# Optimization experiments

Hardware: AMD Instinct MI355X
Metric: run time of the kernel (lower is better)

## Reference

```python
import jax, jax.numpy as jnp
import numpy as np

N_NODES = 50000
N_EDGES = 1_600_000
IN_CH, HID_CH, OUT_CH, EDGE_DIM = 128, 128, 64, 16
NEG_SLOPE = 0.2


def _glorot(key, shape):
    fan = sum(shape) if len(shape) > 1 else shape[0] + 1
    lim = jnp.sqrt(6.0 / fan)
    return jax.random.uniform(key, shape, jnp.float32, -lim, lim)


def setup_inputs() -> dict:
    key = jax.random.key(0)
    ks = jax.random.split(key, 16)
    x = jax.random.normal(ks[0], (N_NODES, IN_CH), jnp.float32)
    edge_index = jax.random.randint(ks[1], (2, N_EDGES), 0, N_NODES, jnp.int32)
    flepe = jax.random.normal(ks[2], (N_EDGES, EDGE_DIM), jnp.float32)
    # layer 1 params (GATConv heads=1)
    W1 = _glorot(ks[3], (IN_CH, HID_CH))
    att_src1 = _glorot(ks[4], (HID_CH,))
    att_dst1 = _glorot(ks[5], (HID_CH,))
    We1 = _glorot(ks[6], (EDGE_DIM, HID_CH))
    att_edge1 = _glorot(ks[7], (HID_CH,))
    b1 = jnp.zeros((HID_CH,), jnp.float32)
    # layer 2 params
    W2 = _glorot(ks[8], (HID_CH, OUT_CH))
    att_src2 = _glorot(ks[9], (OUT_CH,))
    att_dst2 = _glorot(ks[10], (OUT_CH,))
    We2 = _glorot(ks[11], (EDGE_DIM, OUT_CH))
    att_edge2 = _glorot(ks[12], (OUT_CH,))
    b2 = jnp.zeros((OUT_CH,), jnp.float32)
    return {"x": x, "edge_index": edge_index, "flepe": flepe,
            "W1": W1, "att_src1": att_src1, "att_dst1": att_dst1,
            "We1": We1, "att_edge1": att_edge1, "b1": b1,
            "W2": W2, "att_src2": att_src2, "att_dst2": att_dst2,
            "We2": We2, "att_edge2": att_edge2, "b2": b2}


def gat_conv(x, src, dst, edge_attr, W, a_s, a_d, We, a_e, b, n_nodes):
    # PyG GATConv, heads=1, concat=True, negative_slope=0.2, edge_dim set.
    h = x @ W                                    # [N, C]
    alpha_src = h @ a_s                          # [N]
    alpha_dst = h @ a_d                          # [N]
    e = edge_attr @ We                           # [E, C]
    alpha_edge = e @ a_e                         # [E]
    alpha = alpha_src[src] + alpha_dst[dst] + alpha_edge
    alpha = jax.nn.leaky_relu(alpha, NEG_SLOPE)  # [E]
    # segment softmax over incoming edges per destination node
    amax = jax.ops.segment_max(alpha, dst, num_segments=n_nodes)
    amax = jnp.where(jnp.isfinite(amax), amax, 0.0)
    ex = jnp.exp(alpha - amax[dst])
    denom = jax.ops.segment_sum(ex, dst, num_segments=n_nodes)
    coef = ex / (denom[dst] + 1e-16)
    out = jax.ops.segment_sum(coef[:, None] * h[src], dst, num_segments=n_nodes)
    return out + b


def reference(x, edge_index, flepe,
              W1, att_src1, att_dst1, We1, att_edge1, b1,
              W2, att_src2, att_dst2, We2, att_edge2, b2):
    src, dst = edge_index[0], edge_index[1]
    n = x.shape[0]
    # dropout(p=0.5) is identity in eval mode
    h = gat_conv(x, src, dst, flepe, W1, att_src1, att_dst1, We1, att_edge1, b1, n)
    h = jax.nn.relu(h)
    out = gat_conv(h, src, dst, flepe, W2, att_src2, att_dst2, We2, att_edge2, b2, n)
    return out
```

## Files before the change

kernel.cpp:

```cpp
#include <hip/hip_runtime.h>
#include <hip/hip_bf16.h>

typedef unsigned int uint;


__device__ inline float bf2f_lo(uint u) { return __uint_as_float((u & 0xffffu) << 16); }
__device__ inline float bf2f_hi(uint u) { return __uint_as_float(u & 0xffff0000u); }
__device__ inline uint f2bf_rne(float f) {
    uint x = __float_as_uint(f);
    return (x + 0x7fffu + ((x >> 16) & 1u)) >> 16;
}
__device__ inline uint pack_bf2(float a, float b) { return f2bf_rne(a) | (f2bf_rne(b) << 16); }

__global__ void k_deg(const int* __restrict__ dst, int* __restrict__ deg, int E,
                      const float* __restrict__ We1, const float* __restrict__ ae1w,
                      const float* __restrict__ We2, const float* __restrict__ ae2w,
                      float* __restrict__ p1, float* __restrict__ p2) {
    if (blockIdx.x == 0) {
        int t = threadIdx.x;
        if (t < 16) {
            float s = 0.f;
            for (int c = 0; c < 128; ++c) s += We1[t * 128 + c] * ae1w[c];
            p1[t] = s;
        } else if (t < 32) {
            int d = t - 16;
            float s = 0.f;
            for (int c = 0; c < 64; ++c) s += We2[d * 64 + c] * ae2w[c];
            p2[d] = s;
        }
    }
    int e = blockIdx.x * blockDim.x + threadIdx.x;
    if (e < E) atomicAdd(&deg[dst[e]], 1);
}

__global__ __launch_bounds__(1024) void k_scanA(const int* __restrict__ deg,
                                                int* __restrict__ excl,
                                                int* __restrict__ bsum, int N) {
    __shared__ int s[1024];
    int tid = threadIdx.x;
    int gid = blockIdx.x * 1024 + tid;
    int v = (gid < N) ? deg[gid] : 0;
    s[tid] = v;
    __syncthreads();
    for (int off = 1; off < 1024; off <<= 1) {
        int t = (tid >= off) ? s[tid - off] : 0;
        __syncthreads();
        s[tid] += t;
        __syncthreads();
    }
    if (gid < N) excl[gid] = s[tid] - v;
    if (tid == 1023) bsum[blockIdx.x] = s[1023];
}

__global__ void k_scanB(const int* __restrict__ bsum, int* __restrict__ bsumx, int nb,
                        int* __restrict__ rowstart, int N, int E) {
    int t = threadIdx.x;
    int v = (t < nb) ? bsum[t] : 0;
    int x = v;
    for (int o = 1; o < 64; o <<= 1) {
        int y = __shfl_up(x, o);
        if (t >= o) x += y;
    }
    if (t < nb) bsumx[t] = x - v;
    if (t == 0) rowstart[N] = E;
}

__global__ __launch_bounds__(1024) void k_scanC(const int* __restrict__ excl,
                                                const int* __restrict__ bsumx,
                                                int* __restrict__ rowstart,
                                                int* __restrict__ cursor, int N) {
    int gid = blockIdx.x * 1024 + threadIdx.x;
    if (gid < N) {
        int v = excl[gid] + bsumx[blockIdx.x];
        rowstart[gid] = v;
        cursor[gid] = v;
    }
}

__global__ void k_scat(const int* __restrict__ src, const int* __restrict__ dst,
                       const float* __restrict__ fe,
                       const float* __restrict__ p1, const float* __restrict__ p2,
                       int* __restrict__ cursor, float4* __restrict__ rec, int E) {
    float q1[16], q2[16];
#pragma unroll
    for (int i = 0; i < 16; ++i) { q1[i] = p1[i]; q2[i] = p2[i]; }
    int e = blockIdx.x * blockDim.x + threadIdx.x;
    if (e >= E) return;
    int s = src[e], d = dst[e];
    const float4* f = reinterpret_cast<const float4*>(fe) + (size_t)e * 4;
    float a1 = 0.f, a2 = 0.f;
#pragma unroll
    for (int j = 0; j < 4; ++j) {
        float4 v = f[j];
        a1 += v.x * q1[4 * j] + v.y * q1[4 * j + 1] + v.z * q1[4 * j + 2] + v.w * q1[4 * j + 3];
        a2 += v.x * q2[4 * j] + v.y * q2[4 * j + 1] + v.z * q2[4 * j + 2] + v.w * q2[4 * j + 3];
    }
    int pos = atomicAdd(&cursor[d], 1);
    rec[pos] = make_float4(__int_as_float(s), a1, a2, 0.f);
}

template <int COUT>
__global__ __launch_bounds__(256) void k_gemm(
    const float* __restrict__ X, const float* __restrict__ W,
    const float* __restrict__ avs, const float* __restrict__ avd,
    uint* __restrict__ Hb, float* __restrict__ asrc, float* __restrict__ adst, int N) {
    __shared__ float Wl[128 * COUT];
    const int tid = threadIdx.x;
    {
        const float4* W4 = reinterpret_cast<const float4*>(W);
        float4* Wl4 = reinterpret_cast<float4*>(Wl);
        for (int i = tid; i < 128 * COUT / 4; i += 256) Wl4[i] = W4[i];
    }
    __syncthreads();
    const int wv = tid >> 6, lane = tid & 63;
    const int base = __builtin_amdgcn_readfirstlane(blockIdx.x * 32 + wv * 8);

    const float4* xr[8];
#pragma unroll
    for (int r = 0; r < 8; ++r) {
        int g = base + r;
        if (g > N - 1) g = N - 1;
        xr[r] = reinterpret_cast<const float4*>(X + (size_t)g * 128);
    }
    float acc[8][2];
#pragma unroll
    for (int r = 0; r < 8; ++r) { acc[r][0] = 0.f; acc[r][1] = 0.f; }

    for (int k4 = 0; k4 < 32; ++k4) {
        float xv[8][4];
#pragma unroll
        for (int r = 0; r < 8; ++r) {
            float4 t = xr[r][k4];
            xv[r][0] = t.x; xv[r][1] = t.y; xv[r][2] = t.z; xv[r][3] = t.w;
        }
#pragma unroll
        for (int kk = 0; kk < 4; ++kk) {
            int k = 4 * k4 + kk;
            if constexpr (COUT == 128) {
                float2 w2 = *reinterpret_cast<const float2*>(&Wl[k * 128 + 2 * lane]);
#pragma unroll
                for (int r = 0; r < 8; ++r) {
                    acc[r][0] = fmaf(xv[r][kk], w2.x, acc[r][0]);
                    acc[r][1] = fmaf(xv[r][kk], w2.y, acc[r][1]);
                }
            } else {
                float w1 = Wl[k * COUT + lane];
#pragma unroll
                for (int r = 0; r < 8; ++r)
                    acc[r][0] = fmaf(xv[r][kk], w1, acc[r][0]);
            }
        }
    }

#pragma unroll
    for (int r = 0; r < 8; ++r) {
        int g = base + r;
        if (g < N) {
            if constexpr (COUT == 128) {
                Hb[(size_t)g * 64 + lane] = pack_bf2(acc[r][0], acc[r][1]);
                float2 s2 = reinterpret_cast<const float2*>(avs)[lane];
                float2 d2 = reinterpret_cast<const float2*>(avd)[lane];
                float ps = acc[r][0] * s2.x + acc[r][1] * s2.y;
                float pd = acc[r][0] * d2.x + acc[r][1] * d2.y;
                for (int o = 32; o; o >>= 1) { ps += __shfl_xor(ps, o); pd += __shfl_xor(pd, o); }
                if (lane == 0) { asrc[g] = ps; adst[g] = pd; }
            } else {
                float partner = __shfl_xor(acc[r][0], 1);
                if ((lane & 1) == 0)
                    Hb[(size_t)g * 32 + (lane >> 1)] = pack_bf2(acc[r][0], partner);
                float ps = acc[r][0] * avs[lane];
                float pd = acc[r][0] * avd[lane];
                for (int o = 32; o; o >>= 1) { ps += __shfl_xor(ps, o); pd += __shfl_xor(pd, o); }
                if (lane == 0) { asrc[g] = ps; adst[g] = pd; }
            }
        }
    }
}

__global__ __launch_bounds__(256) void k_aggr1(
    const int* __restrict__ rowstart, const float4* __restrict__ rec,
    const float* __restrict__ asrc, const float* __restrict__ adst,
    const uint* __restrict__ Hb, const float* __restrict__ bias,
    float* __restrict__ out, int N) {
    __shared__ uint2 swl[4][64];
    const int wv = threadIdx.x >> 6, lane = threadIdx.x & 63;
    int n = blockIdx.x * 4 + wv;
    if (n >= N) return;
    n = __builtin_amdgcn_readfirstlane(n);
    int s = rowstart[n], e = rowstart[n + 1];
    float ad = adst[n];
    float a0 = 0.f, a1 = 0.f, ws = 0.f;
    for (int base = s; base < e; base += 64) {
        int cnt = e - base; if (cnt > 64) cnt = 64;
        float w = 0.f; int sn = 0;
        if (lane < cnt) {
            float4 rc = rec[base + lane];
            sn = __float_as_int(rc.x);
            float al = asrc[sn] + ad + rc.y;
            al = al > 0.f ? al : 0.2f * al;
            w = __expf(al);
        }
        float wsum = w;
        for (int o = 32; o; o >>= 1) wsum += __shfl_xor(wsum, o);
        ws += wsum;
        swl[wv][lane] = make_uint2((uint)sn, __float_as_uint(w));
        int cnt4 = (cnt + 3) & ~3;
        for (int j = 0; j < cnt4; j += 4) {
            uint2 t0 = swl[wv][j], t1 = swl[wv][j + 1], t2 = swl[wv][j + 2], t3 = swl[wv][j + 3];
            uint h0 = Hb[(size_t)t0.x * 64 + lane];
            uint h1 = Hb[(size_t)t1.x * 64 + lane];
            uint h2 = Hb[(size_t)t2.x * 64 + lane];
            uint h3 = Hb[(size_t)t3.x * 64 + lane];
            float w0 = __uint_as_float(t0.y), w1 = __uint_as_float(t1.y);
            float w2 = __uint_as_float(t2.y), w3 = __uint_as_float(t3.y);
            a0 = fmaf(w0, bf2f_lo(h0), a0); a1 = fmaf(w0, bf2f_hi(h0), a1);
            a0 = fmaf(w1, bf2f_lo(h1), a0); a1 = fmaf(w1, bf2f_hi(h1), a1);
            a0 = fmaf(w2, bf2f_lo(h2), a0); a1 = fmaf(w2, bf2f_hi(h2), a1);
            a0 = fmaf(w3, bf2f_lo(h3), a0); a1 = fmaf(w3, bf2f_hi(h3), a1);
        }
    }
    float inv = 1.0f / (ws + 1e-16f);
    float2 b2 = reinterpret_cast<const float2*>(bias)[lane];
    float o0 = fmaxf(fmaf(a0, inv, b2.x), 0.f);
    float o1 = fmaxf(fmaf(a1, inv, b2.y), 0.f);
    reinterpret_cast<float2*>(out)[(size_t)n * 64 + lane] = make_float2(o0, o1);
}

__global__ __launch_bounds__(256) void k_aggr2(
    const int* __restrict__ rowstart, const float4* __restrict__ rec,
    const float* __restrict__ asrc, const float* __restrict__ adst,
    const uint* __restrict__ Hb, const float* __restrict__ bias,
    float* __restrict__ out, int N) {
    __shared__ uint2 swl[4][64];
    const int wv = threadIdx.x >> 6, lane = threadIdx.x & 63;
    const int half = lane >> 5, hl = lane & 31;
    int n = blockIdx.x * 4 + wv;
    if (n >= N) return;
    n = __builtin_amdgcn_readfirstlane(n);
    int s = rowstart[n], e = rowstart[n + 1];
    float ad = adst[n];
    float a0 = 0.f, a1 = 0.f, ws = 0.f;
    for (int base = s; base < e; base += 64) {
        int cnt = e - base; if (cnt > 64) cnt = 64;
        float w = 0.f; int sn = 0;
        if (lane < cnt) {
            float4 rc = rec[base + lane];
            sn = __float_as_int(rc.x);
            float al = asrc[sn] + ad + rc.z;
            al = al > 0.f ? al : 0.2f * al;
            w = __expf(al);
        }
        float wsum = w;
        for (int o = 32; o; o >>= 1) wsum += __shfl_xor(wsum, o);
        ws += wsum;
        swl[wv][lane] = make_uint2((uint)sn, __float_as_uint(w));
        int cnt4 = (cnt + 3) & ~3;
        for (int j = 0; j < cnt4; j += 4) {
            uint2 t0 = swl[wv][j + half];
            uint2 t1 = swl[wv][j + 2 + half];
            uint h0 = Hb[(size_t)t0.x * 32 + hl];
            uint h1 = Hb[(size_t)t1.x * 32 + hl];
            float w0 = __uint_as_float(t0.y), w1 = __uint_as_float(t1.y);
            a0 = fmaf(w0, bf2f_lo(h0), a0); a1 = fmaf(w0, bf2f_hi(h0), a1);
            a0 = fmaf(w1, bf2f_lo(h1), a0); a1 = fmaf(w1, bf2f_hi(h1), a1);
        }
    }
    a0 += __shfl_xor(a0, 32);
    a1 += __shfl_xor(a1, 32);
    if (half == 0) {
        float inv = 1.0f / (ws + 1e-16f);
        float2 b2 = reinterpret_cast<const float2*>(bias)[hl];
        reinterpret_cast<float2*>(out)[(size_t)n * 32 + hl] =
            make_float2(fmaf(a0, inv, b2.x), fmaf(a1, inv, b2.y));
    }
}

extern "C" void kernel_launch(void* const* d_in, const int* in_sizes, int n_in,
                              void* d_out, int out_size, void* d_ws, size_t ws_size,
                              hipStream_t stream) {
    const float* x    = (const float*)d_in[0];
    const int*   ei   = (const int*)d_in[1];
    const float* fe   = (const float*)d_in[2];
    const float* W1   = (const float*)d_in[3];
    const float* as1  = (const float*)d_in[4];
    const float* ad1  = (const float*)d_in[5];
    const float* We1  = (const float*)d_in[6];
    const float* ae1w = (const float*)d_in[7];
    const float* b1   = (const float*)d_in[8];
    const float* W2   = (const float*)d_in[9];
    const float* as2  = (const float*)d_in[10];
    const float* ad2  = (const float*)d_in[11];
    const float* We2  = (const float*)d_in[12];
    const float* ae2w = (const float*)d_in[13];
    const float* b2   = (const float*)d_in[14];
    float* out = (float*)d_out;

    const int N = in_sizes[0] / 128;
    const int E = in_sizes[1] / 2;
    const int* src = ei;
    const int* dst = ei + E;

    char* ws = (char*)d_ws;
    size_t off = 0;
    auto alloc = [&](size_t bytes) -> void* {
        void* p = ws + off;
        off = (off + bytes + 255) & ~(size_t)255;
        return p;
    };
    float*  p1       = (float*)alloc(64);
    float*  p2       = (float*)alloc(64);
    float4* rec      = (float4*)alloc((size_t)E * 16);
    float*  x2       = (float*)alloc((size_t)N * 128 * 4);
    uint*   H1       = (uint*)alloc((size_t)N * 64 * 4);
    uint*   H2       = (uint*)alloc((size_t)N * 32 * 4);
    float*  asrc     = (float*)alloc((size_t)N * 4);
    float*  adst     = (float*)alloc((size_t)N * 4);
    int*    deg      = (int*)alloc((size_t)N * 4);
    int*    excl     = (int*)alloc((size_t)N * 4);
    int*    rowstart = (int*)alloc((size_t)(N + 1) * 4);
    int*    cursor   = (int*)alloc((size_t)N * 4);
    int*    bsum     = (int*)alloc(256);
    int*    bsumx    = (int*)alloc(256);

    const int nb = (N + 1023) / 1024;

    hipMemsetAsync(deg, 0, (size_t)N * 4, stream);
    k_deg<<<(E + 255) / 256, 256, 0, stream>>>(dst, deg, E, We1, ae1w, We2, ae2w, p1, p2);
    k_scanA<<<nb, 1024, 0, stream>>>(deg, excl, bsum, N);
    k_scanB<<<1, 64, 0, stream>>>(bsum, bsumx, nb, rowstart, N, E);
    k_scanC<<<nb, 1024, 0, stream>>>(excl, bsumx, rowstart, cursor, N);
    k_scat<<<(E + 255) / 256, 256, 0, stream>>>(src, dst, fe, p1, p2, cursor, rec, E);

    k_gemm<128><<<(N + 31) / 32, 256, 0, stream>>>(x, W1, as1, ad1, H1, asrc, adst, N);
    k_aggr1<<<(N + 3) / 4, 256, 0, stream>>>(rowstart, rec, asrc, adst, H1, b1, x2, N);

    k_gemm<64><<<(N + 31) / 32, 256, 0, stream>>>(x2, W2, as2, ad2, H2, asrc, adst, N);
    k_aggr2<<<(N + 3) / 4, 256, 0, stream>>>(rowstart, rec, asrc, adst, H2, b2, out, N);
}
```

Measured before the change: 542.8 us.

## Use bf16 MFMA for node GEMMs and store layer-1 output as bf16

Replaces the scalar fp32 FMA GEMMs with MFMA 16x16x32 bf16 kernels that read pre-swizzled bf16 weight fragments built by a new prep kernel. The attention projections are reduced from the MFMA accumulators. The layer-1 aggregation now writes bf16 instead of fp32, which halves traffic for the intermediate and feeds the second GEMM directly. In exchange the inputs lose precision to bf16. With N=50000, which is a multiple of 16, the tiled rows need no bounds check, but other sizes would read and write past the end.

```diff
diff --git a/kernel.cpp b/kernel.cpp
--- a/kernel.cpp
+++ b/kernel.cpp
@@ -2,6 +2,8 @@
 #include <hip/hip_bf16.h>
 
 typedef unsigned int uint;
+typedef __attribute__((ext_vector_type(8))) short bf16x8;
+typedef __attribute__((ext_vector_type(4))) float f32x4;
 
 
 __device__ inline float bf2f_lo(uint u) { return __uint_as_float((u & 0xffffu) << 16); }
@@ -11,6 +13,31 @@
     return (x + 0x7fffu + ((x >> 16) & 1u)) >> 16;
 }
 __device__ inline uint pack_bf2(float a, float b) { return f2bf_rne(a) | (f2bf_rne(b) << 16); }
+
+__global__ void k_prep(const float* __restrict__ W1, const float* __restrict__ W2,
+                       uint4* __restrict__ S1, uint4* __restrict__ S2) {
+    int t = blockIdx.x * 256 + threadIdx.x;
+    if (t < 2048) {
+        int f = t >> 6, l = t & 63;
+        int kb = f >> 3, cb = f & 7;
+        int k0 = kb * 32 + (l >> 4) * 8, c = cb * 16 + (l & 15);
+        uint u[4];
+#pragma unroll
+        for (int m = 0; m < 4; ++m)
+            u[m] = pack_bf2(W1[(k0 + 2 * m) * 128 + c], W1[(k0 + 2 * m + 1) * 128 + c]);
+        S1[t] = make_uint4(u[0], u[1], u[2], u[3]);
+    } else if (t < 3072) {
+        int tt = t - 2048;
+        int f = tt >> 6, l = tt & 63;
+        int kb = f >> 2, cb = f & 3;
+        int k0 = kb * 32 + (l >> 4) * 8, c = cb * 16 + (l & 15);
+        uint u[4];
+#pragma unroll
+        for (int m = 0; m < 4; ++m)
+            u[m] = pack_bf2(W2[(k0 + 2 * m) * 64 + c], W2[(k0 + 2 * m + 1) * 64 + c]);
+        S2[tt] = make_uint4(u[0], u[1], u[2], u[3]);
+    }
+}
 
 __global__ void k_deg(const int* __restrict__ dst, int* __restrict__ deg, int E,
                       const float* __restrict__ We1, const float* __restrict__ ae1w,
@@ -99,80 +126,89 @@
     rec[pos] = make_float4(__int_as_float(s), a1, a2, 0.f);
 }
 
-template <int COUT>
-__global__ __launch_bounds__(256) void k_gemm(
-    const float* __restrict__ X, const float* __restrict__ W,
+template <int COUT, bool BF16IN>
+__global__ __launch_bounds__(256) void k_gemm_mfma(
+    const void* __restrict__ Xv, const uint4* __restrict__ Wswz,
     const float* __restrict__ avs, const float* __restrict__ avd,
-    uint* __restrict__ Hb, float* __restrict__ asrc, float* __restrict__ adst, int N) {
-    __shared__ float Wl[128 * COUT];
-    const int tid = threadIdx.x;
-    {
-        const float4* W4 = reinterpret_cast<const float4*>(W);
-        float4* Wl4 = reinterpret_cast<float4*>(Wl);
-        for (int i = tid; i < 128 * COUT / 4; i += 256) Wl4[i] = W4[i];
-    }
+    uint* __restrict__ Hb, float* __restrict__ asrc, float* __restrict__ adst,
+    int ntiles) {
+    constexpr int NCB = COUT / 16;
+    constexpr int NFRAG = NCB * 4;
+    __shared__ uint4 WB[NFRAG * 64];
+    for (int i = threadIdx.x; i < NFRAG * 64; i += 256) WB[i] = Wswz[i];
     __syncthreads();
-    const int wv = tid >> 6, lane = tid & 63;
-    const int base = __builtin_amdgcn_readfirstlane(blockIdx.x * 32 + wv * 8);
-
-    const float4* xr[8];
-#pragma unroll
-    for (int r = 0; r < 8; ++r) {
-        int g = base + r;
-        if (g > N - 1) g = N - 1;
-        xr[r] = reinterpret_cast<const float4*>(X + (size_t)g * 128);
-    }
-    float acc[8][2];
-#pragma unroll
-    for (int r = 0; r < 8; ++r) { acc[r][0] = 0.f; acc[r][1] = 0.f; }
-
-    for (int k4 = 0; k4 < 32; ++k4) {
-        float xv[8][4];
-#pragma unroll
-        for (int r = 0; r < 8; ++r) {
-            float4 t = xr[r][k4];
-            xv[r][0] = t.x; xv[r][1] = t.y; xv[r][2] = t.z; xv[r][3] = t.w;
-        }
-#pragma unroll
-        for (int kk = 0; kk < 4; ++kk) {
-            int k = 4 * k4 + kk;
-            if constexpr (COUT == 128) {
-                float2 w2 = *reinterpret_cast<const float2*>(&Wl[k * 128 + 2 * lane]);
-#pragma unroll
-                for (int r = 0; r < 8; ++r) {
-                    acc[r][0] = fmaf(xv[r][kk], w2.x, acc[r][0]);
-                    acc[r][1] = fmaf(xv[r][kk], w2.y, acc[r][1]);
-                }
-            } else {
-                float w1 = Wl[k * COUT + lane];
-#pragma unroll
-                for (int r = 0; r < 8; ++r)
-                    acc[r][0] = fmaf(xv[r][kk], w1, acc[r][0]);
-            }
-        }
-    }
-
-#pragma unroll
-    for (int r = 0; r < 8; ++r) {
-        int g = base + r;
-        if (g < N) {
-            if constexpr (COUT == 128) {
-                Hb[(size_t)g * 64 + lane] = pack_bf2(acc[r][0], acc[r][1]);
-                float2 s2 = reinterpret_cast<const float2*>(avs)[lane];
-                float2 d2 = reinterpret_cast<const float2*>(avd)[lane];
-                float ps = acc[r][0] * s2.x + acc[r][1] * s2.y;
-                float pd = acc[r][0] * d2.x + acc[r][1] * d2.y;
-                for (int o = 32; o; o >>= 1) { ps += __shfl_xor(ps, o); pd += __shfl_xor(pd, o); }
-                if (lane == 0) { asrc[g] = ps; adst[g] = pd; }
-            } else {
-                float partner = __shfl_xor(acc[r][0], 1);
-                if ((lane & 1) == 0)
-                    Hb[(size_t)g * 32 + (lane >> 1)] = pack_bf2(acc[r][0], partner);
-                float ps = acc[r][0] * avs[lane];
-                float pd = acc[r][0] * avd[lane];
-                for (int o = 32; o; o >>= 1) { ps += __shfl_xor(ps, o); pd += __shfl_xor(pd, o); }
-                if (lane == 0) { asrc[g] = ps; adst[g] = pd; }
-            }
+    const int wv = threadIdx.x >> 6, l = threadIdx.x & 63;
+    const int lrow = l & 15, lkq = l >> 4;
+
+    float vs[NCB], vd[NCB];
+#pragma unroll
+    for (int cb = 0; cb < NCB; ++cb) {
+        vs[cb] = avs[cb * 16 + lrow];
+        vd[cb] = avd[cb * 16 + lrow];
+    }
+    union U16 { uint4 q; bf16x8 v; };
+
+    for (int t = blockIdx.x * 4 + wv; t < ntiles; t += gridDim.x * 4) {
+        const int rowb = t * 16;
+        const int r0 = rowb + lrow;
+        bf16x8 a[4];
+        if constexpr (BF16IN) {
+            const uint4* xr4 = reinterpret_cast<const uint4*>(Xv) + (size_t)r0 * 16;
+#pragma unroll
+            for (int kb = 0; kb < 4; ++kb) {
+                U16 cv; cv.q = xr4[kb * 4 + lkq];
+                a[kb] = cv.v;
+            }
+        } else {
+            const float* xr = reinterpret_cast<const float*>(Xv) + (size_t)r0 * 128 + lkq * 8;
+#pragma unroll
+            for (int kb = 0; kb < 4; ++kb) {
+                float4 f0 = *reinterpret_cast<const float4*>(xr + kb * 32);
+                float4 f1 = *reinterpret_cast<const float4*>(xr + kb * 32 + 4);
+                U16 cv;
+                cv.q = make_uint4(pack_bf2(f0.x, f0.y), pack_bf2(f0.z, f0.w),
+                                  pack_bf2(f1.x, f1.y), pack_bf2(f1.z, f1.w));
+                a[kb] = cv.v;
+            }
+        }
+        f32x4 acc[NCB];
+#pragma unroll
+        for (int cb = 0; cb < NCB; ++cb) acc[cb] = (f32x4){0.f, 0.f, 0.f, 0.f};
+#pragma unroll
+        for (int cb = 0; cb < NCB; ++cb) {
+#pragma unroll
+            for (int kb = 0; kb < 4; ++kb) {
+                U16 bu;
+                bu.q = WB[(kb * NCB + cb) * 64 + l];
+                acc[cb] = __builtin_amdgcn_mfma_f32_16x16x32_bf16(a[kb], bu.v, acc[cb], 0, 0, 0);
+            }
+        }
+        float ps[4] = {0.f, 0.f, 0.f, 0.f}, pd[4] = {0.f, 0.f, 0.f, 0.f};
+#pragma unroll
+        for (int cb = 0; cb < NCB; ++cb) {
+#pragma unroll
+            for (int r = 0; r < 4; ++r) {
+                float v = acc[cb][r];
+                ps[r] += v * vs[cb];
+                pd[r] += v * vd[cb];
+                float pv = __shfl_xor(v, 1);
+                if (!(l & 1))
+                    Hb[(size_t)(rowb + lkq * 4 + r) * (COUT / 2) + cb * 8 + (lrow >> 1)] =
+                        pack_bf2(v, pv);
+            }
+        }
+#pragma unroll
+        for (int o = 1; o < 16; o <<= 1) {
+#pragma unroll
+            for (int r = 0; r < 4; ++r) {
+                ps[r] += __shfl_xor(ps[r], o);
+                pd[r] += __shfl_xor(pd[r], o);
+            }
+        }
+        if (lrow == 0) {
+            int rb = rowb + lkq * 4;
+#pragma unroll
+            for (int r = 0; r < 4; ++r) { asrc[rb + r] = ps[r]; adst[rb + r] = pd[r]; }
         }
     }
 }
@@ -181,7 +217,7 @@
     const int* __restrict__ rowstart, const float4* __restrict__ rec,
     const float* __restrict__ asrc, const float* __restrict__ adst,
     const uint* __restrict__ Hb, const float* __restrict__ bias,
-    float* __restrict__ out, int N) {
+    uint* __restrict__ out, int N) {
     __shared__ uint2 swl[4][64];
     const int wv = threadIdx.x >> 6, lane = threadIdx.x & 63;
     int n = blockIdx.x * 4 + wv;
@@ -223,7 +259,7 @@
     float2 b2 = reinterpret_cast<const float2*>(bias)[lane];
     float o0 = fmaxf(fmaf(a0, inv, b2.x), 0.f);
     float o1 = fmaxf(fmaf(a1, inv, b2.y), 0.f);
-    reinterpret_cast<float2*>(out)[(size_t)n * 64 + lane] = make_float2(o0, o1);
+    out[(size_t)n * 64 + lane] = pack_bf2(o0, o1);
 }
 
 __global__ __launch_bounds__(256) void k_aggr2(
@@ -309,8 +345,10 @@
     };
     float*  p1       = (float*)alloc(64);
     float*  p2       = (float*)alloc(64);
+    uint4*  S1       = (uint4*)alloc(2048 * 16);
+    uint4*  S2       = (uint4*)alloc(1024 * 16);
     float4* rec      = (float4*)alloc((size_t)E * 16);
-    float*  x2       = (float*)alloc((size_t)N * 128 * 4);
+    uint*   x2       = (uint*)alloc((size_t)N * 64 * 4);
     uint*   H1       = (uint*)alloc((size_t)N * 64 * 4);
     uint*   H2       = (uint*)alloc((size_t)N * 32 * 4);
     float*  asrc     = (float*)alloc((size_t)N * 4);
@@ -323,17 +361,19 @@
     int*    bsumx    = (int*)alloc(256);
 
     const int nb = (N + 1023) / 1024;
+    const int ntiles = (N + 15) / 16;
 
     hipMemsetAsync(deg, 0, (size_t)N * 4, stream);
+    k_prep<<<12, 256, 0, stream>>>(W1, W2, S1, S2);
     k_deg<<<(E + 255) / 256, 256, 0, stream>>>(dst, deg, E, We1, ae1w, We2, ae2w, p1, p2);
     k_scanA<<<nb, 1024, 0, stream>>>(deg, excl, bsum, N);
     k_scanB<<<1, 64, 0, stream>>>(bsum, bsumx, nb, rowstart, N, E);
     k_scanC<<<nb, 1024, 0, stream>>>(excl, bsumx, rowstart, cursor, N);
     k_scat<<<(E + 255) / 256, 256, 0, stream>>>(src, dst, fe, p1, p2, cursor, rec, E);
 
-    k_gemm<128><<<(N + 31) / 32, 256, 0, stream>>>(x, W1, as1, ad1, H1, asrc, adst, N);
+    k_gemm_mfma<128, false><<<512, 256, 0, stream>>>(x, S1, as1, ad1, H1, asrc, adst, ntiles);
     k_aggr1<<<(N + 3) / 4, 256, 0, stream>>>(rowstart, rec, asrc, adst, H1, b1, x2, N);
 
-    k_gemm<64><<<(N + 31) / 32, 256, 0, stream>>>(x2, W2, as2, ad2, H2, asrc, adst, N);
+    k_gemm_mfma<64, true><<<512, 256, 0, stream>>>(x2, S2, as2, ad2, H2, asrc, adst, ntiles);
     k_aggr2<<<(N + 3) / 4, 256, 0, stream>>>(rowstart, rec, asrc, adst, H2, b2, out, N);
 }
```

Measured after the change: 438.1 us. -19.3%, faster.
